# Kernel tuning notes

Hardware: AMD Instinct MI355X
Metric: run time of the kernel (lower is better)

Reference implementation:

```python
import jax, jax.numpy as jnp
import numpy as np

NUM_CLASS = 20
ALPHA = 1.0
BETA = 1.0
IGNORE = 255


def _fdiff(f, ax):
    """np.gradient/torch.gradient with unit spacing along axis ax (edge_order=1)."""
    n = f.shape[ax]
    sl = lambda a, b: jax.lax.slice_in_dim(f, a, b, axis=ax)
    interior = (sl(2, n) - sl(0, n - 2)) * 0.5
    first = sl(1, 2) - sl(0, 1)
    last = sl(n - 1, n) - sl(n - 2, n - 1)
    return jnp.concatenate([first, interior, last], axis=ax)


def _lga(targets):
    # one-hot over all classes at once: [C, B, D, H, W]
    cls = jnp.arange(NUM_CLASS, dtype=targets.dtype)[:, None, None, None, None]
    oh = (targets[None] == cls).astype(jnp.float32)
    res = jnp.zeros(targets.shape, jnp.float32)
    for ax in (2, 3, 4):  # spatial dims of [C,B,D,H,W]
        res = res + jnp.sum(jnp.abs(_fdiff(oh, ax)), axis=0)
    return res  # [B, D, H, W]


def setup_inputs() -> dict:
    key = jax.random.key(0)
    k1, k2, k3, k4 = jax.random.split(key, 4)
    B, D, H, W = 1, 256, 256, 32
    predictions = jax.random.normal(k1, (B, NUM_CLASS, D, H, W), dtype=jnp.float32)
    targets = jax.random.randint(k2, (B, D, H, W), 0, NUM_CLASS)
    ignore = jax.random.uniform(k3, (B, D, H, W)) < 0.02
    targets = jnp.where(ignore, IGNORE, targets).astype(jnp.int32)
    class_weights = jax.random.uniform(k4, (NUM_CLASS,), dtype=jnp.float32) + 0.1
    return {"predictions": predictions, "targets": targets, "class_weights": class_weights}


def reference(predictions, targets, class_weights):
    targets = targets.astype(jnp.int32)
    valid = targets != IGNORE
    t = jnp.where(valid, targets, 0)
    # weighted CE, reduction='none': -w[t] * log_softmax(pred)[t], 0 at ignore
    logp = jax.nn.log_softmax(predictions, axis=1)
    logp_t = jnp.take_along_axis(logp, t[:, None], axis=1)[:, 0]  # [B,D,H,W]
    w = class_weights[t]
    loss = jnp.where(valid, -w * logp_t, 0.0)
    lga_weights = ALPHA + BETA * _lga(targets)
    num = jnp.sum(loss * lga_weights)
    den = jnp.sum(jnp.where(valid, w, 0.0))
    return num / den
```

## Files before the change

kernel.cpp:

```cpp
#include <hip/hip_runtime.h>

#define NUM_CLASS 20
#define IGNORE_V 255
#define WW 32
#define HH 256
#define DDEPTH 256
#define NVOX (DDEPTH * HH * WW)
#define NBLK 2048

__device__ __forceinline__ float fpair(int a, int b) {
    return (a == b) ? 0.0f : ((a == IGNORE_V || b == IGNORE_V) ? 1.0f : 2.0f);
}

__global__ __launch_bounds__(256) void pal_main(
    const float* __restrict__ pred,
    const int*   __restrict__ tgt,
    const float* __restrict__ cw,
    float2*      __restrict__ partial)
{
    __shared__ float lcw[NUM_CLASS];
    if (threadIdx.x < NUM_CLASS) lcw[threadIdx.x] = cw[threadIdx.x];
    __syncthreads();

    const int gid = blockIdx.x * blockDim.x + threadIdx.x;
    const int v0  = gid * 4;
    const int w0  = v0 & (WW - 1);
    const int h   = (v0 >> 5) & (HH - 1);
    const int d   = v0 >> 13;

    const int4 t4 = *reinterpret_cast<const int4*>(tgt + v0);
    const int t[4] = {t4.x, t4.y, t4.z, t4.w};
    const int tm1 = tgt[v0 - ((w0 != 0) ? 1 : 0)];
    const int tp4 = tgt[v0 + 3 + ((w0 != WW - 4) ? 1 : 0)];
    const int4 tu4 = *reinterpret_cast<const int4*>(tgt + v0 - ((h != 0)          ? WW      : 0));
    const int4 td4 = *reinterpret_cast<const int4*>(tgt + v0 + ((h != HH - 1)     ? WW      : 0));
    const int4 tb4 = *reinterpret_cast<const int4*>(tgt + v0 - ((d != 0)          ? WW * HH : 0));
    const int4 tf4 = *reinterpret_cast<const int4*>(tgt + v0 + ((d != DDEPTH - 1) ? WW * HH : 0));

    const int rot = blockIdx.x % NUM_CLASS;
    float4 x[NUM_CLASS];
    #pragma unroll
    for (int k = 0; k < NUM_CLASS; k++) {
        int c = rot + k; if (c >= NUM_CLASS) c -= NUM_CLASS;
        x[k] = *reinterpret_cast<const float4*>(pred + (size_t)c * NVOX + v0);
    }

    float s[4]  = {0.f, 0.f, 0.f, 0.f};
    float pt[4] = {0.f, 0.f, 0.f, 0.f};
    #pragma unroll
    for (int k = 0; k < NUM_CLASS; k++) {
        int c = rot + k; if (c >= NUM_CLASS) c -= NUM_CLASS;
        const float xx[4] = {x[k].x, x[k].y, x[k].z, x[k].w};
        #pragma unroll
        for (int j = 0; j < 4; j++) {
            s[j] += __expf(xx[j]);
            if (t[j] == c) pt[j] = xx[j];
        }
    }

    const int tu[4] = {tu4.x, tu4.y, tu4.z, tu4.w};
    const int td[4] = {td4.x, td4.y, td4.z, td4.w};
    const int tb[4] = {tb4.x, tb4.y, tb4.z, tb4.w};
    const int tf[4] = {tf4.x, tf4.y, tf4.z, tf4.w};
    const float scH = (h == 0 || h == HH - 1)     ? 1.0f : 0.5f;
    const float scD = (d == 0 || d == DDEPTH - 1) ? 1.0f : 0.5f;

    float num = 0.0f, den = 0.0f;
    #pragma unroll
    for (int j = 0; j < 4; j++) {
        const int tj = t[j];
        if (tj != IGNORE_V) {
            const int wj = w0 + j;
            const int tL = (j > 0) ? t[j-1] : ((w0 == 0)      ? t[0] : tm1);
            const int tR = (j < 3) ? t[j+1] : ((w0 == WW - 4) ? t[3] : tp4);
            const float scW = (wj == 0 || wj == WW - 1) ? 1.0f : 0.5f;
            const float lga = scW * fpair(tL, tR)
                            + scH * fpair(tu[j], td[j])
                            + scD * fpair(tb[j], tf[j]);
            const float wt = lcw[tj];
            num += wt * (__logf(s[j]) - pt[j]) * (1.0f + lga);
            den += wt;
        }
    }

    #pragma unroll
    for (int off = 32; off > 0; off >>= 1) {
        num += __shfl_down(num, off);
        den += __shfl_down(den, off);
    }
    __shared__ float sn[4], sd[4];
    const int lane = threadIdx.x & 63;
    const int wid  = threadIdx.x >> 6;
    if (lane == 0) { sn[wid] = num; sd[wid] = den; }
    __syncthreads();
    if (threadIdx.x == 0)
        partial[blockIdx.x] = make_float2((sn[0] + sn[1]) + (sn[2] + sn[3]),
                                          (sd[0] + sd[1]) + (sd[2] + sd[3]));
}

__global__ __launch_bounds__(256) void pal_final(
    const float2* __restrict__ partial, float* __restrict__ out)
{
    const float4* p4 = reinterpret_cast<const float4*>(partial);
    float num = 0.f, den = 0.f;
    #pragma unroll
    for (int k = 0; k < 4; k++) {
        const float4 f = p4[threadIdx.x + 256 * k];
        num += f.x + f.z;
        den += f.y + f.w;
    }
    #pragma unroll
    for (int off = 32; off > 0; off >>= 1) {
        num += __shfl_down(num, off);
        den += __shfl_down(den, off);
    }
    __shared__ float sn[4], sd[4];
    const int lane = threadIdx.x & 63;
    const int wid  = threadIdx.x >> 6;
    if (lane == 0) { sn[wid] = num; sd[wid] = den; }
    __syncthreads();
    if (threadIdx.x == 0)
        out[0] = ((sn[0] + sn[1]) + (sn[2] + sn[3])) /
                 ((sd[0] + sd[1]) + (sd[2] + sd[3]));
}

extern "C" void kernel_launch(void* const* d_in, const int* in_sizes, int n_in,
                              void* d_out, int out_size, void* d_ws, size_t ws_size,
                              hipStream_t stream) {
    const float* pred = (const float*)d_in[0];
    const int*   tgt  = (const int*)d_in[1];
    const float* cw   = (const float*)d_in[2];
    float*  out     = (float*)d_out;
    float2* partial = (float2*)d_ws;

    pal_main<<<NBLK, 256, 0, stream>>>(pred, tgt, cw, partial);
    pal_final<<<1, 256, 0, stream>>>(partial, out);
}
```

Before: 250.2 us.

## Stage prediction tiles into LDS via direct global-to-LDS loads in two phases

Instead of each thread loading all 20 class float4 values into registers, each wave issues global_load_lds 16-byte transfers for half of the classes into a 40KB shared buffer. Threads then read from LDS and accumulate, and the process repeats for the second half. This cuts register pressure and is meant to improve memory-level parallelism, but it adds barriers, LDS traffic and a reduced occupancy limit from LDS usage. The per-block class rotation is removed.

Result: faster. 241.9 us (-3.3%).

```diff
diff --git a/kernel.cpp b/kernel.cpp
--- a/kernel.cpp
+++ b/kernel.cpp
@@ -6,10 +6,19 @@
 #define HH 256
 #define DDEPTH 256
 #define NVOX (DDEPTH * HH * WW)
-#define NBLK 2048
+#define CHUNK 1024
+#define NBLK (NVOX / CHUNK)
+#define HALF 10
 
 __device__ __forceinline__ float fpair(int a, int b) {
     return (a == b) ? 0.0f : ((a == IGNORE_V || b == IGNORE_V) ? 1.0f : 2.0f);
+}
+
+__device__ __forceinline__ void stage16(const float* gsrc, float* ldst) {
+    __builtin_amdgcn_global_load_lds(
+        (const __attribute__((address_space(1))) void*)gsrc,
+        (__attribute__((address_space(3))) void*)ldst,
+        16, 0, 0);
 }
 
 __global__ __launch_bounds__(256) void pal_main(
@@ -18,15 +27,18 @@
     const float* __restrict__ cw,
     float2*      __restrict__ partial)
 {
+    __shared__ __align__(16) float lbuf[HALF * CHUNK];
     __shared__ float lcw[NUM_CLASS];
     if (threadIdx.x < NUM_CLASS) lcw[threadIdx.x] = cw[threadIdx.x];
-    __syncthreads();
 
-    const int gid = blockIdx.x * blockDim.x + threadIdx.x;
-    const int v0  = gid * 4;
-    const int w0  = v0 & (WW - 1);
-    const int h   = (v0 >> 5) & (HH - 1);
-    const int d   = v0 >> 13;
+    const int tid   = threadIdx.x;
+    const int lane  = tid & 63;
+    const int wid   = tid >> 6;
+    const int base  = blockIdx.x * CHUNK;
+    const int v0    = base + tid * 4;
+    const int w0    = v0 & (WW - 1);
+    const int h     = (v0 >> 5) & (HH - 1);
+    const int d     = v0 >> 13;
 
     const int4 t4 = *reinterpret_cast<const int4*>(tgt + v0);
     const int t[4] = {t4.x, t4.y, t4.z, t4.w};
@@ -37,25 +49,32 @@
     const int4 tb4 = *reinterpret_cast<const int4*>(tgt + v0 - ((d != 0)          ? WW * HH : 0));
     const int4 tf4 = *reinterpret_cast<const int4*>(tgt + v0 + ((d != DDEPTH - 1) ? WW * HH : 0));
 
-    const int rot = blockIdx.x % NUM_CLASS;
-    float4 x[NUM_CLASS];
-    #pragma unroll
-    for (int k = 0; k < NUM_CLASS; k++) {
-        int c = rot + k; if (c >= NUM_CLASS) c -= NUM_CLASS;
-        x[k] = *reinterpret_cast<const float4*>(pred + (size_t)c * NVOX + v0);
-    }
-
+    const int woff = wid * 256;
+    const float* gwave = pred + base + woff + lane * 4;
     float s[4]  = {0.f, 0.f, 0.f, 0.f};
     float pt[4] = {0.f, 0.f, 0.f, 0.f};
+
     #pragma unroll
-    for (int k = 0; k < NUM_CLASS; k++) {
-        int c = rot + k; if (c >= NUM_CLASS) c -= NUM_CLASS;
-        const float xx[4] = {x[k].x, x[k].y, x[k].z, x[k].w};
+    for (int ph = 0; ph < 2; ph++) {
+        const int cs = ph * HALF;
         #pragma unroll
-        for (int j = 0; j < 4; j++) {
-            s[j] += __expf(xx[j]);
-            if (t[j] == c) pt[j] = xx[j];
+        for (int k = 0; k < HALF; k++)
+            stage16(gwave + (size_t)(cs + k) * NVOX, lbuf + k * CHUNK + woff);
+        __syncthreads();
+
+        const float* lp = lbuf + tid * 4;
+        #pragma unroll
+        for (int k = 0; k < HALF; k++) {
+            const float4 x = *reinterpret_cast<const float4*>(lp + k * CHUNK);
+            const int c = cs + k;
+            const float xx[4] = {x.x, x.y, x.z, x.w};
+            #pragma unroll
+            for (int j = 0; j < 4; j++) {
+                s[j] += __expf(xx[j]);
+                if (t[j] == c) pt[j] = xx[j];
+            }
         }
+        __syncthreads();
     }
 
     const int tu[4] = {tu4.x, tu4.y, tu4.z, tu4.w};
@@ -89,11 +108,9 @@
         den += __shfl_down(den, off);
     }
     __shared__ float sn[4], sd[4];
-    const int lane = threadIdx.x & 63;
-    const int wid  = threadIdx.x >> 6;
     if (lane == 0) { sn[wid] = num; sd[wid] = den; }
     __syncthreads();
-    if (threadIdx.x == 0)
+    if (tid == 0)
         partial[blockIdx.x] = make_float2((sn[0] + sn[1]) + (sn[2] + sn[3]),
                                           (sd[0] + sd[1]) + (sd[2] + sd[3]));
 }
```
